# Kernel optimization log

Hardware: AMD Instinct MI355X
Metric: run time of the kernel (lower is better)

Reference implementation:

```python
import jax, jax.numpy as jnp
import numpy as np

N_NODES = 50000
N_EDGES = 800000
DIM = 128
N_LAYERS = 5
BN_EPS = 1e-3  # keras BatchNormalization default epsilon


def setup_inputs() -> dict:
    key = jax.random.key(0)
    ks = jax.random.split(key, 6)
    scale = 1.0 / np.sqrt(DIM)
    return {
        "x": jax.random.normal(ks[0], (N_NODES, DIM), dtype=jnp.float32),
        "edge_src": jax.random.randint(ks[1], (N_EDGES,), 0, N_NODES, dtype=jnp.int32),
        "edge_dst": jax.random.randint(ks[2], (N_EDGES,), 0, N_NODES, dtype=jnp.int32),
        "eps": jnp.zeros((N_LAYERS,), dtype=jnp.float32),
        "W1": jax.random.normal(ks[3], (N_LAYERS, DIM, DIM), dtype=jnp.float32) * scale,
        "b1": jnp.zeros((N_LAYERS, DIM), dtype=jnp.float32),
        "W2": jax.random.normal(ks[4], (N_LAYERS, DIM, DIM), dtype=jnp.float32) * scale,
        "b2": jnp.zeros((N_LAYERS, DIM), dtype=jnp.float32),
        "gamma": jnp.ones((N_LAYERS, DIM), dtype=jnp.float32),
        "beta": jnp.zeros((N_LAYERS, DIM), dtype=jnp.float32),
        "bn_mean": jnp.zeros((N_LAYERS, DIM), dtype=jnp.float32),
        "bn_var": jnp.ones((N_LAYERS, DIM), dtype=jnp.float32),
    }


def reference(x, edge_src, edge_dst, eps, W1, b1, W2, b2, gamma, beta, bn_mean, bn_var):
    n = x.shape[0]
    num_layers = W1.shape[0]
    hidden_rep = [x]
    h = x
    for l in range(num_layers):
        # sparse Adj @ h as gather + segment-sum (sum neighbor pooling)
        msgs = jnp.take(h, edge_src, axis=0)                       # [E, D]
        pooled = jax.ops.segment_sum(msgs, edge_dst, num_segments=n)  # [N, D]
        pooled = pooled + (1.0 + eps[l]) * h                        # GIN eps term
        # 2-layer MLP: Linear -> ReLU -> Linear
        z = jax.nn.relu(pooled @ W1[l] + b1[l])
        z = z @ W2[l] + b2[l]
        # BatchNorm (inference: moving statistics)
        z = gamma[l] * (z - bn_mean[l]) * jax.lax.rsqrt(bn_var[l] + BN_EPS) + beta[l]
        h = jax.nn.relu(z)
        hidden_rep.append(h)
    return tuple(hidden_rep)
```

## Files before the change

### kernel.cpp

```cpp
#include <hip/hip_runtime.h>
#include <hip/hip_bf16.h>

#define N_NODES 50000
#define N_EDGES 800000
#define DIM 128
#define N_LAYERS 5
#define BN_EPS 1e-3f
#define NBLK_SCAN ((N_NODES + 255) / 256)

typedef __attribute__((ext_vector_type(8))) short bf16x8;
typedef __attribute__((ext_vector_type(4))) float f32x4;
typedef __attribute__((ext_vector_type(4))) unsigned int u32x4;
typedef __attribute__((ext_vector_type(2))) unsigned int u32x2;

__device__ __forceinline__ unsigned short f2bf(float f) {
    unsigned int v = __builtin_bit_cast(unsigned int, f);
    v += 0x7fffu + ((v >> 16) & 1u);
    return (unsigned short)(v >> 16);
}
__device__ __forceinline__ float bflo(unsigned int v) {
    return __builtin_bit_cast(float, v << 16);
}
__device__ __forceinline__ float bfhi(unsigned int v) {
    return __builtin_bit_cast(float, v & 0xffff0000u);
}


__global__ void init_zero_kernel(const float* __restrict__ x, float* __restrict__ out,
                                 unsigned short* __restrict__ hb, int* __restrict__ cnt) {
    int t = blockIdx.x * blockDim.x + threadIdx.x;
    if (t < (N_NODES * DIM) / 4) {
        f32x4 v = ((const f32x4*)x)[t];
        __builtin_nontemporal_store(v, (f32x4*)out + t);
        unsigned short u[4] = {f2bf(v.x), f2bf(v.y), f2bf(v.z), f2bf(v.w)};
        *(u32x2*)(hb + t * 4) = *(u32x2*)u;
    }
    int z = t - (N_NODES * DIM) / 4;
    if (z >= 0 && z < N_NODES) cnt[z] = 0;
}

__global__ void hist_kernel(const int* __restrict__ dst, int* __restrict__ cnt) {
    int e = blockIdx.x * blockDim.x + threadIdx.x;
    if (e < N_EDGES) atomicAdd(&cnt[dst[e]], 1);
}

__global__ __launch_bounds__(256) void scanA_kernel(const int* __restrict__ cnt,
                                                    int* __restrict__ blocksum) {
    const int tid = threadIdx.x, lane = tid & 63, wave = tid >> 6;
    int i = blockIdx.x * 256 + tid;
    int v = (i < N_NODES) ? cnt[i] : 0;
#pragma unroll
    for (int off = 1; off < 64; off <<= 1) v += __shfl_xor(v, off, 64);
    __shared__ int ws[4];
    if (lane == 0) ws[wave] = v;
    __syncthreads();
    if (tid == 0) blocksum[blockIdx.x] = ws[0] + ws[1] + ws[2] + ws[3];
}

__global__ __launch_bounds__(256) void scanB_kernel(int* __restrict__ blocksum,
                                                    int* __restrict__ row_start) {
    __shared__ int s[256];
    const int tid = threadIdx.x;
    int v = (tid < NBLK_SCAN) ? blocksum[tid] : 0;
    s[tid] = v;
    __syncthreads();
#pragma unroll
    for (int off = 1; off < 256; off <<= 1) {
        int t = (tid >= off) ? s[tid - off] : 0;
        __syncthreads();
        s[tid] += t;
        __syncthreads();
    }
    if (tid < NBLK_SCAN) blocksum[tid] = s[tid] - v;
    if (tid == 0) row_start[N_NODES] = N_EDGES;
}

__global__ __launch_bounds__(256) void scanC_kernel(const int* __restrict__ cnt,
                                                    const int* __restrict__ blockoff,
                                                    int* __restrict__ row_start,
                                                    int* __restrict__ cursor) {
    const int tid = threadIdx.x, lane = tid & 63, wave = tid >> 6;
    int i = blockIdx.x * 256 + tid;
    int v = (i < N_NODES) ? cnt[i] : 0;
    int x = v;
#pragma unroll
    for (int off = 1; off < 64; off <<= 1) {
        int t = __shfl_up(x, off, 64);
        if (lane >= off) x += t;
    }
    __shared__ int ws[4];
    if (lane == 63) ws[wave] = x;
    __syncthreads();
    int woff = 0;
    if (wave > 0) woff += ws[0];
    if (wave > 1) woff += ws[1];
    if (wave > 2) woff += ws[2];
    int excl = blockoff[blockIdx.x] + woff + x - v;
    if (i < N_NODES) { row_start[i] = excl; cursor[i] = excl; }
}

__global__ void fill_kernel(const int* __restrict__ src, const int* __restrict__ dst,
                            int* __restrict__ cursor, int* __restrict__ col) {
    int e = blockIdx.x * blockDim.x + threadIdx.x;
    if (e < N_EDGES) {
        int d = dst[e];
        int pos = atomicAdd(&cursor[d], 1);
        col[pos] = src[e];
    }
}

__global__ void prep_kernel(const float* __restrict__ W1, const float* __restrict__ W2,
                            unsigned short* __restrict__ wp,
                            const float* __restrict__ gamma, const float* __restrict__ beta,
                            const float* __restrict__ mean, const float* __restrict__ var,
                            float* __restrict__ scale, float* __restrict__ shift) {
    int t = blockIdx.x * blockDim.x + threadIdx.x;
    if (t < N_LAYERS * 2 * 2048) {
        int mat = t >> 11;
        int r = t & 2047;
        int ks = r >> 9, nt = (r >> 6) & 7, lane = r & 63;
        int layer = mat >> 1;
        const float* W = ((mat & 1) ? W2 : W1) + layer * DIM * DIM;
        int n = nt * 16 + (lane & 15);
        int kb = ks * 32 + (lane >> 4) * 8;
        unsigned short u[8];
#pragma unroll
        for (int j = 0; j < 8; j++) u[j] = f2bf(W[(kb + j) * DIM + n]);
        *(u32x4*)(wp + (size_t)mat * 16384 + ((ks * 8 + nt) * 64 + lane) * 8) = *(u32x4*)u;
    }
    int i = t - N_LAYERS * 2 * 2048;
    if (i >= 0 && i < N_LAYERS * DIM) {
        float sc = gamma[i] * rsqrtf(var[i] + BN_EPS);
        scale[i] = sc;
        shift[i] = beta[i] - mean[i] * sc;
    }
}


__global__ __launch_bounds__(256) void pool_kernel(const unsigned short* __restrict__ hb,
                                                   const int* __restrict__ row_start,
                                                   const int* __restrict__ col,
                                                   const float* __restrict__ eps_l,
                                                   unsigned short* __restrict__ pooled_b) {
    const int wave = threadIdx.x >> 6, lane = threadIdx.x & 63;
    const int n = blockIdx.x * 4 + wave;
    if (n >= N_NODES) return;
    const float ev = 1.0f + eps_l[0];
    const int s0 = row_start[n], s1 = row_start[n + 1];
    const int c2 = lane * 2;

    unsigned int sv = *(const unsigned int*)(hb + n * DIM + c2);
    float a0 = ev * bflo(sv);
    float a1 = ev * bfhi(sv);

    for (int base = s0; base < s1; base += 64) {
        const int nn = (s1 - base < 64) ? (s1 - base) : 64;
        int ci = (base + lane < s1) ? col[base + lane] : 0;
        for (int j = 0; j < nn; j += 8) {
            int s[8];
            unsigned int v[8];
#pragma unroll
            for (int q = 0; q < 8; q++) s[q] = __shfl(ci, j + q, 64);
#pragma unroll
            for (int q = 0; q < 8; q++)
                v[q] = *(const unsigned int*)(hb + s[q] * DIM + c2);
#pragma unroll
            for (int q = 0; q < 8; q++) {
                if (j + q < nn) { a0 += bflo(v[q]); a1 += bfhi(v[q]); }
            }
        }
    }
    unsigned short u[2] = {f2bf(a0), f2bf(a1)};
    *(unsigned int*)(pooled_b + n * DIM + c2) = *(unsigned int*)u;
}

__global__ __launch_bounds__(256) void mlp_kernel(
    const unsigned short* __restrict__ pooled_b,
    const unsigned short* __restrict__ wp1,
    const unsigned short* __restrict__ wp2,
    const float* __restrict__ b1,
    const float* __restrict__ b2,
    const float* __restrict__ bnscale,
    const float* __restrict__ bnshift,
    float* __restrict__ h_out,
    unsigned short* __restrict__ hb_out) {
    __shared__ __align__(16) unsigned short zfrag[4][4][64][8];
    const int tid = threadIdx.x;
    const int wave = tid >> 6, lane = tid & 63;
    const int m0 = blockIdx.x * 64;
    const int colc = lane & 15;
    const int quad = lane >> 4;
    const int arow = m0 + wave * 16 + colc;
    const int arow_c = arow < N_NODES ? arow : N_NODES - 1;

    bf16x8 a[4];
#pragma unroll
    for (int ks = 0; ks < 4; ks++)
        a[ks] = *(const bf16x8*)(pooled_b + arow_c * DIM + ks * 32 + quad * 8);

    f32x4 acc[8];
#pragma unroll
    for (int nt = 0; nt < 8; nt++) {
        acc[nt] = (f32x4){0.f, 0.f, 0.f, 0.f};
#pragma unroll
        for (int ks = 0; ks < 4; ks++) {
            bf16x8 b = *(const bf16x8*)(wp1 + ((ks * 8 + nt) * 64 + lane) * 8);
            acc[nt] = __builtin_amdgcn_mfma_f32_16x16x32_bf16(a[ks], b, acc[nt], 0, 0, 0);
        }
    }

#pragma unroll
    for (int nt = 0; nt < 8; nt++) {
        int n = nt * 16 + colc;
        float bias = b1[n];
#pragma unroll
        for (int r = 0; r < 4; r++) {
            float v = acc[nt][r] + bias;
            v = v > 0.f ? v : 0.f;
            int row16 = quad * 4 + r;
            zfrag[wave][n >> 5][(((n >> 3) & 3) << 4) | row16][n & 7] = f2bf(v);
        }
    }

#pragma unroll
    for (int ks = 0; ks < 4; ks++) a[ks] = *(const bf16x8*)(&zfrag[wave][ks][lane][0]);

    f32x4 acc2[8];
#pragma unroll
    for (int nt = 0; nt < 8; nt++) {
        acc2[nt] = (f32x4){0.f, 0.f, 0.f, 0.f};
#pragma unroll
        for (int ks = 0; ks < 4; ks++) {
            bf16x8 b = *(const bf16x8*)(wp2 + ((ks * 8 + nt) * 64 + lane) * 8);
            acc2[nt] = __builtin_amdgcn_mfma_f32_16x16x32_bf16(a[ks], b, acc2[nt], 0, 0, 0);
        }
    }

#pragma unroll
    for (int nt = 0; nt < 8; nt++) {
        int n = nt * 16 + colc;
        float bias = b2[n];
        float sc = bnscale[n], sh = bnshift[n];
#pragma unroll
        for (int r = 0; r < 4; r++) {
            int row = m0 + wave * 16 + quad * 4 + r;
            if (row < N_NODES) {
                float z = acc2[nt][r] + bias;
                z = z * sc + sh;
                z = z > 0.f ? z : 0.f;
                __builtin_nontemporal_store(z, &h_out[row * DIM + n]);
                hb_out[row * DIM + n] = f2bf(z);
            }
        }
    }
}


extern "C" void kernel_launch(void* const* d_in, const int* in_sizes, int n_in,
                              void* d_out, int out_size, void* d_ws, size_t ws_size,
                              hipStream_t stream) {
    const float* x     = (const float*)d_in[0];
    const int* esrc    = (const int*)d_in[1];
    const int* edst    = (const int*)d_in[2];
    const float* eps   = (const float*)d_in[3];
    const float* W1    = (const float*)d_in[4];
    const float* b1    = (const float*)d_in[5];
    const float* W2    = (const float*)d_in[6];
    const float* b2    = (const float*)d_in[7];
    const float* gam   = (const float*)d_in[8];
    const float* bet   = (const float*)d_in[9];
    const float* bmean = (const float*)d_in[10];
    const float* bvar  = (const float*)d_in[11];
    float* out = (float*)d_out;

    char* ws = (char*)d_ws;
    unsigned short* hb0   = (unsigned short*)(ws);
    unsigned short* hb1   = (unsigned short*)(ws + 12800000);
    int*   col        = (int*)  (ws + 25600000);
    int*   row_start  = (int*)  (ws + 28800000);
    int*   cursor     = (int*)  (ws + 29000192);
    int*   cnt        = (int*)  (ws + 29200384);
    int*   blocksum   = (int*)  (ws + 29400576);
    unsigned short* wpack = (unsigned short*)(ws + 29401600);
    float* bnscale    = (float*)(ws + 29729280);
    float* bnshift    = (float*)(ws + 29731840);
    unsigned short* pooled_b = (unsigned short*)(ws + 29734400);

    init_zero_kernel<<<((N_NODES * DIM) / 4 + N_NODES + 255) / 256, 256, 0, stream>>>(
        x, out, hb0, cnt);
    hist_kernel<<<(N_EDGES + 255) / 256, 256, 0, stream>>>(edst, cnt);
    scanA_kernel<<<NBLK_SCAN, 256, 0, stream>>>(cnt, blocksum);
    scanB_kernel<<<1, 256, 0, stream>>>(blocksum, row_start);
    scanC_kernel<<<NBLK_SCAN, 256, 0, stream>>>(cnt, blocksum, row_start, cursor);
    fill_kernel<<<(N_EDGES + 255) / 256, 256, 0, stream>>>(esrc, edst, cursor, col);
    prep_kernel<<<(N_LAYERS * 2 * 2048 + N_LAYERS * DIM + 255) / 256, 256, 0, stream>>>(
        W1, W2, wpack, gam, bet, bmean, bvar, bnscale, bnshift);

    const int pool_blocks = (N_NODES + 3) / 4;
    const int mlp_blocks  = (N_NODES + 63) / 64;
    unsigned short* hbuf[2] = {hb0, hb1};
    for (int l = 0; l < N_LAYERS; l++) {
        float* h_next = out + (size_t)(l + 1) * N_NODES * DIM;
        pool_kernel<<<pool_blocks, 256, 0, stream>>>(hbuf[l & 1], row_start, col, eps + l,
                                                     pooled_b);
        mlp_kernel<<<mlp_blocks, 256, 0, stream>>>(
            pooled_b,
            wpack + (size_t)(l * 2) * 16384,
            wpack + (size_t)(l * 2 + 1) * 16384,
            b1 + l * DIM, b2 + l * DIM,
            bnscale + l * DIM, bnshift + l * DIM,
            h_next, hbuf[(l + 1) & 1]);
    }
}
```

Baseline: 537.8 us.

## Bucket CSR by source range and process gather buckets in phases across persistent waves

Result: slower. 616.0 us (+14.6%).

```diff
diff --git a/kernel.cpp b/kernel.cpp
--- a/kernel.cpp
+++ b/kernel.cpp
@@ -6,7 +6,12 @@
 #define DIM 128
 #define N_LAYERS 5
 #define BN_EPS 1e-3f
-#define NBLK_SCAN ((N_NODES + 255) / 256)
+#define KBUK 4
+#define BUCKET 12500
+#define NB2 (N_NODES * KBUK)
+#define NBLK2 ((NB2 + 255) / 256)
+#define POOL_WAVES 8192
+#define NPW 7
 
 typedef __attribute__((ext_vector_type(8))) short bf16x8;
 typedef __attribute__((ext_vector_type(4))) float f32x4;
@@ -27,7 +32,7 @@
 
 
 __global__ void init_zero_kernel(const float* __restrict__ x, float* __restrict__ out,
-                                 unsigned short* __restrict__ hb, int* __restrict__ cnt) {
+                                 unsigned short* __restrict__ hb, int* __restrict__ cnt2) {
     int t = blockIdx.x * blockDim.x + threadIdx.x;
     if (t < (N_NODES * DIM) / 4) {
         f32x4 v = ((const f32x4*)x)[t];
@@ -36,19 +41,23 @@
         *(u32x2*)(hb + t * 4) = *(u32x2*)u;
     }
     int z = t - (N_NODES * DIM) / 4;
-    if (z >= 0 && z < N_NODES) cnt[z] = 0;
-}
-
-__global__ void hist_kernel(const int* __restrict__ dst, int* __restrict__ cnt) {
+    if (z >= 0 && z < NB2) cnt2[z] = 0;
+}
+
+__global__ void hist_kernel(const int* __restrict__ src, const int* __restrict__ dst,
+                            int* __restrict__ cnt2) {
     int e = blockIdx.x * blockDim.x + threadIdx.x;
-    if (e < N_EDGES) atomicAdd(&cnt[dst[e]], 1);
-}
-
-__global__ __launch_bounds__(256) void scanA_kernel(const int* __restrict__ cnt,
+    if (e < N_EDGES) {
+        int b = src[e] / BUCKET;
+        atomicAdd(&cnt2[dst[e] * KBUK + b], 1);
+    }
+}
+
+__global__ __launch_bounds__(256) void scanA_kernel(const int* __restrict__ cnt2,
                                                     int* __restrict__ blocksum) {
     const int tid = threadIdx.x, lane = tid & 63, wave = tid >> 6;
     int i = blockIdx.x * 256 + tid;
-    int v = (i < N_NODES) ? cnt[i] : 0;
+    int v = (i < NB2) ? cnt2[i] : 0;
 #pragma unroll
     for (int off = 1; off < 64; off <<= 1) v += __shfl_xor(v, off, 64);
     __shared__ int ws[4];
@@ -57,31 +66,31 @@
     if (tid == 0) blocksum[blockIdx.x] = ws[0] + ws[1] + ws[2] + ws[3];
 }
 
-__global__ __launch_bounds__(256) void scanB_kernel(int* __restrict__ blocksum,
-                                                    int* __restrict__ row_start) {
-    __shared__ int s[256];
+__global__ __launch_bounds__(1024) void scanB_kernel(int* __restrict__ blocksum,
+                                                     int* __restrict__ rs2) {
+    __shared__ int s[1024];
     const int tid = threadIdx.x;
-    int v = (tid < NBLK_SCAN) ? blocksum[tid] : 0;
+    int v = (tid < NBLK2) ? blocksum[tid] : 0;
     s[tid] = v;
     __syncthreads();
 #pragma unroll
-    for (int off = 1; off < 256; off <<= 1) {
+    for (int off = 1; off < 1024; off <<= 1) {
         int t = (tid >= off) ? s[tid - off] : 0;
         __syncthreads();
         s[tid] += t;
         __syncthreads();
     }
-    if (tid < NBLK_SCAN) blocksum[tid] = s[tid] - v;
-    if (tid == 0) row_start[N_NODES] = N_EDGES;
-}
-
-__global__ __launch_bounds__(256) void scanC_kernel(const int* __restrict__ cnt,
+    if (tid < NBLK2) blocksum[tid] = s[tid] - v;
+    if (tid == 0) rs2[NB2] = N_EDGES;
+}
+
+__global__ __launch_bounds__(256) void scanC_kernel(const int* __restrict__ cnt2,
                                                     const int* __restrict__ blockoff,
-                                                    int* __restrict__ row_start,
-                                                    int* __restrict__ cursor) {
+                                                    int* __restrict__ rs2,
+                                                    int* __restrict__ cursor2) {
     const int tid = threadIdx.x, lane = tid & 63, wave = tid >> 6;
     int i = blockIdx.x * 256 + tid;
-    int v = (i < N_NODES) ? cnt[i] : 0;
+    int v = (i < NB2) ? cnt2[i] : 0;
     int x = v;
 #pragma unroll
     for (int off = 1; off < 64; off <<= 1) {
@@ -96,16 +105,17 @@
     if (wave > 1) woff += ws[1];
     if (wave > 2) woff += ws[2];
     int excl = blockoff[blockIdx.x] + woff + x - v;
-    if (i < N_NODES) { row_start[i] = excl; cursor[i] = excl; }
+    if (i < NB2) { rs2[i] = excl; cursor2[i] = excl; }
 }
 
 __global__ void fill_kernel(const int* __restrict__ src, const int* __restrict__ dst,
-                            int* __restrict__ cursor, int* __restrict__ col) {
+                            int* __restrict__ cursor2, int* __restrict__ col) {
     int e = blockIdx.x * blockDim.x + threadIdx.x;
     if (e < N_EDGES) {
-        int d = dst[e];
-        int pos = atomicAdd(&cursor[d], 1);
-        col[pos] = src[e];
+        int s = src[e];
+        int b = s / BUCKET;
+        int pos = atomicAdd(&cursor2[dst[e] * KBUK + b], 1);
+        col[pos] = s;
     }
 }
 
@@ -138,40 +148,69 @@
 
 
 __global__ __launch_bounds__(256) void pool_kernel(const unsigned short* __restrict__ hb,
-                                                   const int* __restrict__ row_start,
+                                                   const int* __restrict__ rs2,
                                                    const int* __restrict__ col,
                                                    const float* __restrict__ eps_l,
                                                    unsigned short* __restrict__ pooled_b) {
     const int wave = threadIdx.x >> 6, lane = threadIdx.x & 63;
-    const int n = blockIdx.x * 4 + wave;
-    if (n >= N_NODES) return;
+    const int wid = blockIdx.x * 4 + wave;
     const float ev = 1.0f + eps_l[0];
-    const int s0 = row_start[n], s1 = row_start[n + 1];
     const int c2 = lane * 2;
 
-    unsigned int sv = *(const unsigned int*)(hb + n * DIM + c2);
-    float a0 = ev * bflo(sv);
-    float a1 = ev * bfhi(sv);
-
-    for (int base = s0; base < s1; base += 64) {
-        const int nn = (s1 - base < 64) ? (s1 - base) : 64;
-        int ci = (base + lane < s1) ? col[base + lane] : 0;
-        for (int j = 0; j < nn; j += 8) {
-            int s[8];
-            unsigned int v[8];
-#pragma unroll
-            for (int q = 0; q < 8; q++) s[q] = __shfl(ci, j + q, 64);
-#pragma unroll
-            for (int q = 0; q < 8; q++)
-                v[q] = *(const unsigned int*)(hb + s[q] * DIM + c2);
-#pragma unroll
-            for (int q = 0; q < 8; q++) {
-                if (j + q < nn) { a0 += bflo(v[q]); a1 += bfhi(v[q]); }
+    float a0[NPW], a1[NPW];
+#pragma unroll
+    for (int i = 0; i < NPW; i++) {
+        int n = wid + POOL_WAVES * i;
+        if (n < N_NODES) {
+            unsigned int sv = *(const unsigned int*)(hb + (size_t)n * DIM + c2);
+            a0[i] = ev * bflo(sv);
+            a1[i] = ev * bfhi(sv);
+        } else {
+            a0[i] = 0.f; a1[i] = 0.f;
+        }
+    }
+
+    for (int k = 0; k < KBUK; k++) {
+#pragma unroll
+        for (int i = 0; i < NPW; i++) {
+            int n = wid + POOL_WAVES * i;
+            if (n < N_NODES) {
+                const int e0 = rs2[n * KBUK + k], e1 = rs2[n * KBUK + k + 1];
+                for (int base = e0; base < e1; base += 64) {
+                    const int nn = (e1 - base < 64) ? (e1 - base) : 64;
+                    int idx = base + lane;
+                    idx = idx < e1 - 1 ? idx : e1 - 1;
+                    int ci = col[idx];
+                    for (int j = 0; j < nn; j += 4) {
+                        int s[4];
+                        unsigned int v[4];
+#pragma unroll
+                        for (int q = 0; q < 4; q++) {
+                            int jj = j + q;
+                            jj = jj < nn - 1 ? jj : nn - 1;
+                            s[q] = __shfl(ci, jj, 64);
+                        }
+#pragma unroll
+                        for (int q = 0; q < 4; q++)
+                            v[q] = *(const unsigned int*)(hb + (size_t)s[q] * DIM + c2);
+#pragma unroll
+                        for (int q = 0; q < 4; q++) {
+                            if (j + q < nn) { a0[i] += bflo(v[q]); a1[i] += bfhi(v[q]); }
+                        }
+                    }
+                }
             }
         }
     }
-    unsigned short u[2] = {f2bf(a0), f2bf(a1)};
-    *(unsigned int*)(pooled_b + n * DIM + c2) = *(unsigned int*)u;
+
+#pragma unroll
+    for (int i = 0; i < NPW; i++) {
+        int n = wid + POOL_WAVES * i;
+        if (n < N_NODES) {
+            unsigned short u[2] = {f2bf(a0[i]), f2bf(a1[i])};
+            *(unsigned int*)(pooled_b + (size_t)n * DIM + c2) = *(unsigned int*)u;
+        }
+    }
 }
 
 __global__ __launch_bounds__(256) void mlp_kernel(
@@ -277,31 +316,31 @@
     unsigned short* hb0   = (unsigned short*)(ws);
     unsigned short* hb1   = (unsigned short*)(ws + 12800000);
     int*   col        = (int*)  (ws + 25600000);
-    int*   row_start  = (int*)  (ws + 28800000);
-    int*   cursor     = (int*)  (ws + 29000192);
-    int*   cnt        = (int*)  (ws + 29200384);
-    int*   blocksum   = (int*)  (ws + 29400576);
-    unsigned short* wpack = (unsigned short*)(ws + 29401600);
-    float* bnscale    = (float*)(ws + 29729280);
-    float* bnshift    = (float*)(ws + 29731840);
-    unsigned short* pooled_b = (unsigned short*)(ws + 29734400);
-
-    init_zero_kernel<<<((N_NODES * DIM) / 4 + N_NODES + 255) / 256, 256, 0, stream>>>(
-        x, out, hb0, cnt);
-    hist_kernel<<<(N_EDGES + 255) / 256, 256, 0, stream>>>(edst, cnt);
-    scanA_kernel<<<NBLK_SCAN, 256, 0, stream>>>(cnt, blocksum);
-    scanB_kernel<<<1, 256, 0, stream>>>(blocksum, row_start);
-    scanC_kernel<<<NBLK_SCAN, 256, 0, stream>>>(cnt, blocksum, row_start, cursor);
-    fill_kernel<<<(N_EDGES + 255) / 256, 256, 0, stream>>>(esrc, edst, cursor, col);
+    int*   rs2        = (int*)  (ws + 28800000);
+    int*   cursor2    = (int*)  (ws + 29600256);
+    int*   cnt2       = (int*)  (ws + 30400256);
+    int*   blocksum   = (int*)  (ws + 31200256);
+    unsigned short* wpack = (unsigned short*)(ws + 31203584);
+    float* bnscale    = (float*)(ws + 31531264);
+    float* bnshift    = (float*)(ws + 31533824);
+    unsigned short* pooled_b = (unsigned short*)(ws + 31536384);
+
+    init_zero_kernel<<<((N_NODES * DIM) / 4 + NB2 + 255) / 256, 256, 0, stream>>>(
+        x, out, hb0, cnt2);
+    hist_kernel<<<(N_EDGES + 255) / 256, 256, 0, stream>>>(esrc, edst, cnt2);
+    scanA_kernel<<<NBLK2, 256, 0, stream>>>(cnt2, blocksum);
+    scanB_kernel<<<1, 1024, 0, stream>>>(blocksum, rs2);
+    scanC_kernel<<<NBLK2, 256, 0, stream>>>(cnt2, blocksum, rs2, cursor2);
+    fill_kernel<<<(N_EDGES + 255) / 256, 256, 0, stream>>>(esrc, edst, cursor2, col);
     prep_kernel<<<(N_LAYERS * 2 * 2048 + N_LAYERS * DIM + 255) / 256, 256, 0, stream>>>(
         W1, W2, wpack, gam, bet, bmean, bvar, bnscale, bnshift);
 
-    const int pool_blocks = (N_NODES + 3) / 4;
+    const int pool_blocks = POOL_WAVES / 4;
     const int mlp_blocks  = (N_NODES + 63) / 64;
     unsigned short* hbuf[2] = {hb0, hb1};
     for (int l = 0; l < N_LAYERS; l++) {
         float* h_next = out + (size_t)(l + 1) * N_NODES * DIM;
-        pool_kernel<<<pool_blocks, 256, 0, stream>>>(hbuf[l & 1], row_start, col, eps + l,
+        pool_kernel<<<pool_blocks, 256, 0, stream>>>(hbuf[l & 1], rs2, col, eps + l,
                                                      pooled_b);
         mlp_kernel<<<mlp_blocks, 256, 0, stream>>>(
             pooled_b,
```

## Fuse neighbor pooling and MLP into one per-layer kernel via LDS

Applied to the files above, without the earlier changes.

Result: faster. 509.4 us (-5.3%).

```diff
diff --git a/kernel.cpp b/kernel.cpp
--- a/kernel.cpp
+++ b/kernel.cpp
@@ -136,46 +136,11 @@
     }
 }
 
-
-__global__ __launch_bounds__(256) void pool_kernel(const unsigned short* __restrict__ hb,
-                                                   const int* __restrict__ row_start,
-                                                   const int* __restrict__ col,
-                                                   const float* __restrict__ eps_l,
-                                                   unsigned short* __restrict__ pooled_b) {
-    const int wave = threadIdx.x >> 6, lane = threadIdx.x & 63;
-    const int n = blockIdx.x * 4 + wave;
-    if (n >= N_NODES) return;
-    const float ev = 1.0f + eps_l[0];
-    const int s0 = row_start[n], s1 = row_start[n + 1];
-    const int c2 = lane * 2;
-
-    unsigned int sv = *(const unsigned int*)(hb + n * DIM + c2);
-    float a0 = ev * bflo(sv);
-    float a1 = ev * bfhi(sv);
-
-    for (int base = s0; base < s1; base += 64) {
-        const int nn = (s1 - base < 64) ? (s1 - base) : 64;
-        int ci = (base + lane < s1) ? col[base + lane] : 0;
-        for (int j = 0; j < nn; j += 8) {
-            int s[8];
-            unsigned int v[8];
-#pragma unroll
-            for (int q = 0; q < 8; q++) s[q] = __shfl(ci, j + q, 64);
-#pragma unroll
-            for (int q = 0; q < 8; q++)
-                v[q] = *(const unsigned int*)(hb + s[q] * DIM + c2);
-#pragma unroll
-            for (int q = 0; q < 8; q++) {
-                if (j + q < nn) { a0 += bflo(v[q]); a1 += bfhi(v[q]); }
-            }
-        }
-    }
-    unsigned short u[2] = {f2bf(a0), f2bf(a1)};
-    *(unsigned int*)(pooled_b + n * DIM + c2) = *(unsigned int*)u;
-}
-
-__global__ __launch_bounds__(256) void mlp_kernel(
-    const unsigned short* __restrict__ pooled_b,
+__global__ __launch_bounds__(1024) void layer_kernel(
+    const unsigned short* __restrict__ hb,
+    const int* __restrict__ row_start,
+    const int* __restrict__ col,
+    const float* __restrict__ eps_l,
     const unsigned short* __restrict__ wp1,
     const unsigned short* __restrict__ wp2,
     const float* __restrict__ b1,
@@ -183,73 +148,116 @@
     const float* __restrict__ bnscale,
     const float* __restrict__ bnshift,
     float* __restrict__ h_out,
-    unsigned short* __restrict__ hb_out) {
+    unsigned short* __restrict__ hb_out,
+    const int store_hb) {
+    __shared__ unsigned int pooled[64 * 64];
     __shared__ __align__(16) unsigned short zfrag[4][4][64][8];
     const int tid = threadIdx.x;
     const int wave = tid >> 6, lane = tid & 63;
     const int m0 = blockIdx.x * 64;
-    const int colc = lane & 15;
-    const int quad = lane >> 4;
-    const int arow = m0 + wave * 16 + colc;
-    const int arow_c = arow < N_NODES ? arow : N_NODES - 1;
+    const float ev = 1.0f + eps_l[0];
+
+    for (int i = 0; i < 4; i++) {
+        const int lrow = wave * 4 + i;
+        const int n = m0 + lrow;
+        float a0 = 0.f, a1 = 0.f;
+        if (n < N_NODES) {
+            unsigned int sv = *(const unsigned int*)(hb + (size_t)n * DIM + lane * 2);
+            a0 = ev * bflo(sv);
+            a1 = ev * bfhi(sv);
+            const int s0 = row_start[n], s1 = row_start[n + 1];
+            for (int base = s0; base < s1; base += 64) {
+                const int nn = (s1 - base < 64) ? (s1 - base) : 64;
+                int ci = (base + lane < s1) ? col[base + lane] : 0;
+                for (int j = 0; j < nn; j += 8) {
+                    int s[8];
+                    unsigned int v[8];
+#pragma unroll
+                    for (int q = 0; q < 8; q++) s[q] = __shfl(ci, j + q, 64);
+#pragma unroll
+                    for (int q = 0; q < 8; q++)
+                        v[q] = *(const unsigned int*)(hb + (size_t)s[q] * DIM + lane * 2);
+#pragma unroll
+                    for (int q = 0; q < 8; q++) {
+                        if (j + q < nn) { a0 += bflo(v[q]); a1 += bfhi(v[q]); }
+                    }
+                }
+            }
+        }
+        unsigned short u[2] = {f2bf(a0), f2bf(a1)};
+        int g = (lane >> 2) ^ (lrow & 15);
+        pooled[lrow * 64 + (g << 2) + (lane & 3)] = *(unsigned int*)u;
+    }
+    __syncthreads();
+
+    const int r = wave >> 2, c = wave & 3;
+    const int colc = lane & 15, quad = lane >> 4;
+    const int lr = r * 16 + colc;
 
     bf16x8 a[4];
 #pragma unroll
-    for (int ks = 0; ks < 4; ks++)
-        a[ks] = *(const bf16x8*)(pooled_b + arow_c * DIM + ks * 32 + quad * 8);
-
-    f32x4 acc[8];
-#pragma unroll
-    for (int nt = 0; nt < 8; nt++) {
-        acc[nt] = (f32x4){0.f, 0.f, 0.f, 0.f};
+    for (int ks = 0; ks < 4; ks++) {
+        int g = (ks * 4 + quad) ^ (lr & 15);
+        a[ks] = *(const bf16x8*)(&pooled[lr * 64 + (g << 2)]);
+    }
+
+    f32x4 acc[2];
+#pragma unroll
+    for (int q = 0; q < 2; q++) {
+        const int nt = c * 2 + q;
+        acc[q] = (f32x4){0.f, 0.f, 0.f, 0.f};
 #pragma unroll
         for (int ks = 0; ks < 4; ks++) {
             bf16x8 b = *(const bf16x8*)(wp1 + ((ks * 8 + nt) * 64 + lane) * 8);
-            acc[nt] = __builtin_amdgcn_mfma_f32_16x16x32_bf16(a[ks], b, acc[nt], 0, 0, 0);
-        }
-    }
-
-#pragma unroll
-    for (int nt = 0; nt < 8; nt++) {
-        int n = nt * 16 + colc;
+            acc[q] = __builtin_amdgcn_mfma_f32_16x16x32_bf16(a[ks], b, acc[q], 0, 0, 0);
+        }
+    }
+
+#pragma unroll
+    for (int q = 0; q < 2; q++) {
+        const int nt = c * 2 + q;
+        const int n = nt * 16 + colc;
         float bias = b1[n];
 #pragma unroll
-        for (int r = 0; r < 4; r++) {
-            float v = acc[nt][r] + bias;
+        for (int rr = 0; rr < 4; rr++) {
+            float v = acc[q][rr] + bias;
             v = v > 0.f ? v : 0.f;
-            int row16 = quad * 4 + r;
-            zfrag[wave][n >> 5][(((n >> 3) & 3) << 4) | row16][n & 7] = f2bf(v);
-        }
-    }
-
-#pragma unroll
-    for (int ks = 0; ks < 4; ks++) a[ks] = *(const bf16x8*)(&zfrag[wave][ks][lane][0]);
-
-    f32x4 acc2[8];
-#pragma unroll
-    for (int nt = 0; nt < 8; nt++) {
-        acc2[nt] = (f32x4){0.f, 0.f, 0.f, 0.f};
+            int row16 = quad * 4 + rr;
+            zfrag[r][n >> 5][(((n >> 3) & 3) << 4) | row16][n & 7] = f2bf(v);
+        }
+    }
+    __syncthreads();
+
+#pragma unroll
+    for (int ks = 0; ks < 4; ks++) a[ks] = *(const bf16x8*)(&zfrag[r][ks][lane][0]);
+
+    f32x4 acc2[2];
+#pragma unroll
+    for (int q = 0; q < 2; q++) {
+        const int nt = c * 2 + q;
+        acc2[q] = (f32x4){0.f, 0.f, 0.f, 0.f};
 #pragma unroll
         for (int ks = 0; ks < 4; ks++) {
             bf16x8 b = *(const bf16x8*)(wp2 + ((ks * 8 + nt) * 64 + lane) * 8);
-            acc2[nt] = __builtin_amdgcn_mfma_f32_16x16x32_bf16(a[ks], b, acc2[nt], 0, 0, 0);
-        }
-    }
-
-#pragma unroll
-    for (int nt = 0; nt < 8; nt++) {
-        int n = nt * 16 + colc;
+            acc2[q] = __builtin_amdgcn_mfma_f32_16x16x32_bf16(a[ks], b, acc2[q], 0, 0, 0);
+        }
+    }
+
+#pragma unroll
+    for (int q = 0; q < 2; q++) {
+        const int nt = c * 2 + q;
+        const int n = nt * 16 + colc;
         float bias = b2[n];
         float sc = bnscale[n], sh = bnshift[n];
 #pragma unroll
-        for (int r = 0; r < 4; r++) {
-            int row = m0 + wave * 16 + quad * 4 + r;
+        for (int rr = 0; rr < 4; rr++) {
+            int row = m0 + r * 16 + quad * 4 + rr;
             if (row < N_NODES) {
-                float z = acc2[nt][r] + bias;
+                float z = acc2[q][rr] + bias;
                 z = z * sc + sh;
                 z = z > 0.f ? z : 0.f;
-                __builtin_nontemporal_store(z, &h_out[row * DIM + n]);
-                hb_out[row * DIM + n] = f2bf(z);
+                __builtin_nontemporal_store(z, &h_out[(size_t)row * DIM + n]);
+                if (store_hb) hb_out[(size_t)row * DIM + n] = f2bf(z);
             }
         }
     }
@@ -284,7 +292,6 @@
     unsigned short* wpack = (unsigned short*)(ws + 29401600);
     float* bnscale    = (float*)(ws + 29729280);
     float* bnshift    = (float*)(ws + 29731840);
-    unsigned short* pooled_b = (unsigned short*)(ws + 29734400);
 
     init_zero_kernel<<<((N_NODES * DIM) / 4 + N_NODES + 255) / 256, 256, 0, stream>>>(
         x, out, hb0, cnt);
@@ -296,19 +303,17 @@
     prep_kernel<<<(N_LAYERS * 2 * 2048 + N_LAYERS * DIM + 255) / 256, 256, 0, stream>>>(
         W1, W2, wpack, gam, bet, bmean, bvar, bnscale, bnshift);
 
-    const int pool_blocks = (N_NODES + 3) / 4;
-    const int mlp_blocks  = (N_NODES + 63) / 64;
+    const int layer_blocks = (N_NODES + 63) / 64;
     unsigned short* hbuf[2] = {hb0, hb1};
     for (int l = 0; l < N_LAYERS; l++) {
         float* h_next = out + (size_t)(l + 1) * N_NODES * DIM;
-        pool_kernel<<<pool_blocks, 256, 0, stream>>>(hbuf[l & 1], row_start, col, eps + l,
-                                                     pooled_b);
-        mlp_kernel<<<mlp_blocks, 256, 0, stream>>>(
-            pooled_b,
+        layer_kernel<<<layer_blocks, 1024, 0, stream>>>(
+            hbuf[l & 1], row_start, col, eps + l,
             wpack + (size_t)(l * 2) * 16384,
             wpack + (size_t)(l * 2 + 1) * 16384,
             b1 + l * DIM, b2 + l * DIM,
             bnscale + l * DIM, bnshift + l * DIM,
-            h_next, hbuf[(l + 1) & 1]);
-    }
-}
+            h_next, hbuf[(l + 1) & 1],
+            (l + 1 < N_LAYERS) ? 1 : 0);
+    }
+}
```
